# Kernel tuning notes

Measured on AMD Instinct MI355X. Metric: run time of the kernel, lower is better.

Reference implementation:

```python
import jax, jax.numpy as jnp
import numpy as np

B, N_HEADS, F_TOK = 8, 12, 768
GRID_H, GRID_W = 32, 32
N_TOK = 1 + GRID_H * GRID_W  # 1025 (readout token + patches)
F_HEAD = F_TOK // N_HEADS    # 64
NUM_DIST = (2 * GRID_H - 1) * (2 * GRID_W - 1) + 3  # 3972


def _build_relpos_index(gh, gw):
    # BEiT-style relative position index with 3 extra slots for the readout token
    coords = np.stack(np.meshgrid(np.arange(gh), np.arange(gw), indexing='ij'))  # (2, gh, gw)
    flat = coords.reshape(2, -1)                                                 # (2, gh*gw)
    rel = flat[:, :, None] - flat[:, None, :]                                    # (2, P, P)
    rel = rel.transpose(1, 2, 0).astype(np.int64)                                # (P, P, 2)
    rel[:, :, 0] += gh - 1
    rel[:, :, 1] += gw - 1
    rel[:, :, 0] *= 2 * gw - 1
    rpi = rel.sum(-1)                                                            # (P, P)
    n = 1 + gh * gw
    nd = (2 * gh - 1) * (2 * gw - 1) + 3
    idx = np.zeros((n, n), dtype=np.int32)
    idx[1:, 1:] = rpi
    idx[0, :] = nd - 3  # readout -> all
    idx[:, 0] = nd - 2  # all -> readout
    idx[0, 0] = nd - 1  # readout -> readout
    return idx


def setup_inputs() -> dict:
    key = jax.random.key(0)
    ks = jax.random.split(key, 7)
    tokens = jax.random.normal(ks[0], (B, N_TOK, F_TOK), dtype=jnp.float32)
    qkv_w = jax.random.normal(ks[1], (3 * F_TOK, F_TOK), dtype=jnp.float32) * 0.02
    q_bias = jax.random.normal(ks[2], (1, N_HEADS, 1, F_HEAD), dtype=jnp.float32) * 0.02
    v_bias = jax.random.normal(ks[3], (1, N_HEADS, 1, F_HEAD), dtype=jnp.float32) * 0.02
    relpos_table = jax.random.normal(ks[4], (NUM_DIST, N_HEADS), dtype=jnp.float32) * 0.02
    proj_w = jax.random.normal(ks[5], (F_TOK, F_TOK), dtype=jnp.float32) * 0.02
    proj_b = jax.random.normal(ks[6], (F_TOK,), dtype=jnp.float32) * 0.02
    relpos_index = jnp.asarray(_build_relpos_index(GRID_H, GRID_W))  # (N, N) int32
    return {
        'tokens': tokens, 'qkv_w': qkv_w, 'q_bias': q_bias, 'v_bias': v_bias,
        'relpos_table': relpos_table, 'proj_w': proj_w, 'proj_b': proj_b,
        'relpos_index': relpos_index, 'patch_h': GRID_H, 'patch_w': GRID_W,
    }


def reference(tokens, qkv_w, q_bias, v_bias, relpos_table, proj_w, proj_b,
              relpos_index, patch_h, patch_w):
    b, n, f_tok = tokens.shape
    # qkv projection (no bias): (B, N, 3F) -> (3, B, H, N, f)
    qkv = tokens @ qkv_w.T
    qkv = qkv.reshape(b, n, 3, N_HEADS, F_HEAD).transpose(2, 0, 3, 1, 4)
    q, k, v = qkv[0], qkv[1], qkv[2]
    q = (q + q_bias) * (F_HEAD ** -0.5)
    v = v + v_bias
    # attention scores: (B, H, N, N)
    attn = jnp.einsum('bhnf,bhmf->bhnm', q, k)
    # relative position bias gather: (N, N, H) -> (H, N, N)
    bias = relpos_table[relpos_index].transpose(2, 0, 1)
    attn = attn + bias[None]
    w = jax.nn.softmax(attn, axis=-1)
    out = jnp.einsum('bhnm,bhmf->bhnf', w, v)
    out = out.transpose(0, 2, 1, 3).reshape(b, n, N_HEADS * F_HEAD)
    return out @ proj_w.T + proj_b
```

## Files before the change

kernel.cpp:

```cpp
#include <hip/hip_runtime.h>

#define B_ 8
#define NH 12
#define NTOK 1025
#define FT 768
#define MROWS (B_*NTOK)
#define QPAD 1025
#define CH2 34
#define NQT 36
#define NTT 34
#define NDIST 3972
#define LOG2E 1.44269504089f

typedef __bf16 bf16x8 __attribute__((ext_vector_type(8)));
typedef __bf16 bf16x2 __attribute__((ext_vector_type(2)));
typedef float floatx4 __attribute__((ext_vector_type(4)));
typedef float floatx16 __attribute__((ext_vector_type(16)));
typedef int intx4 __attribute__((ext_vector_type(4)));

__device__ __forceinline__ void async_ld16(const void* gp, void* lp) {
  __builtin_amdgcn_global_load_lds(
      (const __attribute__((address_space(1))) void*)gp,
      (__attribute__((address_space(3))) void*)lp, 16, 0, 0);
}

__global__ __launch_bounds__(256) void cvt_bf16(const float* __restrict__ src,
                                                __bf16* __restrict__ dst, int n4) {
  int i = blockIdx.x * 256 + threadIdx.x;
  if (i >= n4) return;
  float4 v = ((const float4*)src)[i];
  __bf16 o[4] = {(__bf16)v.x, (__bf16)v.y, (__bf16)v.z, (__bf16)v.w};
  *(uint2*)(dst + 4 * (size_t)i) = *(uint2*)o;
}

__global__ __launch_bounds__(256) void table_prep(const float* __restrict__ table,
                                                  __bf16* __restrict__ tableT) {
  int i = blockIdx.x * 256 + threadIdx.x;
  if (i >= NH * NDIST) return;
  int h = i / NDIST, d = i - h * NDIST;
  tableT[i] = (__bf16)(table[(size_t)d * NH + h] * LOG2E);
}

__global__ __launch_bounds__(256) void bias_gather_t(
    const int* __restrict__ idx, const __bf16* __restrict__ tableT,
    __bf16* __restrict__ Bb) {
  __shared__ int ids_l[32][33];
  const int qt = blockIdx.x, tt = blockIdx.y;
  const int t = threadIdx.x;
  {
    const int row = t >> 3, c4 = (t & 7) * 4;
    int qrow = qt * 32 + row; if (qrow > NTOK - 1) qrow = NTOK - 1;
    const int* src = idx + (size_t)qrow * NTOK;
#pragma unroll
    for (int j = 0; j < 4; ++j) {
      int token = tt * 32 + c4 + j; if (token > NTOK - 1) token = NTOK - 1;
      ids_l[row][c4 + j] = src[token];
    }
  }
  __syncthreads();
  const int lane = t & 63, w = t >> 6;
  const int l31 = lane & 31, hb = lane >> 5;
  int ids[16]; bool ok[16];
#pragma unroll
  for (int j = 0; j < 16; ++j) {
    const int col = (j & 3) + 8 * (j >> 2) + 4 * hb;
    ok[j] = tt * 32 + col < NTOK;
    ids[j] = ids_l[l31][col];
  }
#pragma unroll
  for (int g = 0; g < 3; ++g) {
    const int h = w + g * 4;
    const __bf16* tb = tableT + (size_t)h * NDIST;
    __bf16 v[16] __attribute__((aligned(16)));
#pragma unroll
    for (int j = 0; j < 16; ++j)
      v[j] = ok[j] ? tb[ids[j]] : (__bf16)(-1e30f);
    uint4* dst = (uint4*)(Bb + (((size_t)h * NQT + qt) * NTT + tt) * 1024 + lane * 16);
    dst[0] = ((uint4*)v)[0];
    dst[1] = ((uint4*)v)[1];
  }
}

__device__ __forceinline__ void gemm256_pipe(
    const __bf16* __restrict__ A, const __bf16* __restrict__ W,
    int am0, int n0, __bf16* Lt, floatx4 acc[4][4]) {
  const int tid = threadIdx.x, wave = tid >> 6, lane = tid & 63;
  const int l = lane & 15, qd = lane >> 4;
  const int srow = lane >> 2, sg = lane & 3;
  const int swb = (sg ^ (srow & 3)) * 8;
  const int wr = wave >> 1, wc = wave & 1;

  const __bf16* gsrc[3];
  int gdst[3];
#pragma unroll
  for (int i = 0; i < 3; ++i) {
    const int g = wave * 3 + i;
    if (g < 16) {
      int row = am0 + g * 16 + srow; if (row > MROWS - 1) row = MROWS - 1;
      gsrc[i] = A + (size_t)row * FT + swb;
      gdst[i] = g * 512;
    } else {
      const int row = n0 + (g - 16) * 16 + srow;
      gsrc[i] = W + (size_t)row * FT + swb;
      gdst[i] = 8192 + (g - 16) * 512;
    }
  }
  const int fsw = (qd ^ (l & 3)) * 8;

  auto issue = [&](int k, int buf) {
    __bf16* base = Lt + buf * 12288;
#pragma unroll
    for (int i = 0; i < 3; ++i)
      async_ld16(gsrc[i] + k * 32, base + gdst[i]);
  };
  auto step = [&](int buf) {
    __builtin_amdgcn_s_barrier();
    const __bf16* ab = Lt + buf * 12288;
    const __bf16* bb = ab + 8192;
    bf16x8 aF[4], bF[4];
#pragma unroll
    for (int t = 0; t < 4; ++t)
      aF[t] = *(const bf16x8*)(ab + (wr * 64 + t * 16 + l) * 32 + fsw);
#pragma unroll
    for (int u = 0; u < 4; ++u)
      bF[u] = *(const bf16x8*)(bb + (wc * 64 + u * 16 + l) * 32 + fsw);
#pragma unroll
    for (int t = 0; t < 4; ++t)
#pragma unroll
      for (int u = 0; u < 4; ++u)
        acc[t][u] = __builtin_amdgcn_mfma_f32_16x16x32_bf16(aF[t], bF[u], acc[t][u], 0, 0, 0);
  };

  issue(0, 0);
  int b0 = 0;
  for (int k = 0; k < 24; ++k) {
    if (k < 23) {
      int b1 = b0 + 1; if (b1 == 3) b1 = 0;
      issue(k + 1, b1);
      __builtin_amdgcn_s_waitcnt(0x0F73);
    } else {
      __builtin_amdgcn_s_waitcnt(0x0F70);
    }
    step(b0);
    ++b0; if (b0 == 3) b0 = 0;
  }
}

__global__ __launch_bounds__(512, 4) void qkv_gemm256(
    const __bf16* __restrict__ tokens, const __bf16* __restrict__ qkvw,
    const float* __restrict__ qbias, const float* __restrict__ vbias,
    __bf16* __restrict__ Qb, __bf16* __restrict__ Kc, __bf16* __restrict__ Vc) {
  __shared__ __bf16 Lt[3 * 12288];
  const int u0 = blockIdx.x;
  const int c = u0 & 7, i0 = u0 >> 3;
  const int base = (c < 2) ? c * 75 : 150 + (c - 2) * 74;
  const int w = base + i0;
  const int mt = w / 18, ni = w % 18;
  const int am0 = mt * 256, n0 = ni * 128;
  const int tid = threadIdx.x, wave = tid >> 6, lane = tid & 63;
  const int l = lane & 15, qd = lane >> 4;
  const int wr = wave >> 1, wc = wave & 1;
  floatx4 acc[4][4];
#pragma unroll
  for (int t = 0; t < 4; ++t)
#pragma unroll
    for (int u = 0; u < 4; ++u) acc[t][u] = (floatx4){0.f, 0.f, 0.f, 0.f};
  gemm256_pipe(tokens, qkvw, am0, n0, Lt, acc);

  const int which = ni / 6;
  const int nrem0 = (ni - which * 6) * 128;
#pragma unroll
  for (int u = 0; u < 4; ++u) {
    const int rem = nrem0 + wc * 64 + u * 16 + l;
    const int h = rem >> 6, f = rem & 63;
    const float qb = (which == 0) ? qbias[h * 64 + f] : 0.f;
    const float vb = (which == 2) ? vbias[h * 64 + f] : 0.f;
#pragma unroll
    for (int t = 0; t < 4; ++t) {
      const int gmb = am0 + wr * 64 + t * 16 + qd * 4;
#pragma unroll
      for (int r = 0; r < 4; ++r) {
        const int gm = gmb + r;
        if (gm >= MROWS) continue;
        const int b = (int)(((unsigned)gm * 16369u) >> 24);
        const int tok = gm - b * 1025;
        const size_t bh = (size_t)(b * NH + h);
        const float v = acc[t][u][r];
        if (which == 0) {
          Qb[(bh * QPAD + tok) * 64 + f] = (__bf16)((v + qb) * (0.125f * LOG2E));
        } else if (which == 1) {
          const size_t e = (bh * CH2 + (tok >> 5)) * 2048 +
                           (f >> 3) * 256 + (tok & 31) * 8 + (f & 7);
          Kc[e] = (__bf16)v;
        } else {
          const size_t e = (bh * CH2 + (tok >> 5)) * 2048 +
                           (((tok >> 3) & 3) * 64 + f) * 8 + (tok & 7);
          Vc[e] = (__bf16)(v + vb);
        }
      }
    }
  }
}

__global__ __launch_bounds__(512, 4) void proj_gemm256(
    const __bf16* __restrict__ Ao, const __bf16* __restrict__ projw,
    const float* __restrict__ projb, float* __restrict__ out) {
  __shared__ __bf16 Lt[3 * 12288];
  const int u0 = blockIdx.x;
  const int c = u0 & 7, i0 = u0 >> 3;
  const int base = (c < 6) ? c * 25 : 150 + (c - 6) * 24;
  const int w = base + i0;
  const int mt = w / 6, ni = w % 6;
  const int am0 = mt * 256, n0 = ni * 128;
  const int tid = threadIdx.x, wave = tid >> 6, lane = tid & 63;
  const int l = lane & 15, qd = lane >> 4;
  const int wr = wave >> 1, wc = wave & 1;
  floatx4 acc[4][4];
#pragma unroll
  for (int t = 0; t < 4; ++t)
#pragma unroll
    for (int u = 0; u < 4; ++u) acc[t][u] = (floatx4){0.f, 0.f, 0.f, 0.f};
  gemm256_pipe(Ao, projw, am0, n0, Lt, acc);

#pragma unroll
  for (int u = 0; u < 4; ++u) {
    const int gn = n0 + wc * 64 + u * 16 + l;
    const float pb = projb[gn];
#pragma unroll
    for (int t = 0; t < 4; ++t) {
      const int gmb = am0 + wr * 64 + t * 16 + qd * 4;
#pragma unroll
      for (int r = 0; r < 4; ++r) {
        const int gm = gmb + r;
        if (gm < MROWS) out[(size_t)gm * FT + gn] = acc[t][u][r] + pb;
      }
    }
  }
}

__global__ __launch_bounds__(256) void attn_flash(
    const __bf16* __restrict__ Qb, const __bf16* __restrict__ Kc,
    const __bf16* __restrict__ Vc, const __bf16* __restrict__ Bb,
    __bf16* __restrict__ Ao) {
  __shared__ __bf16 Kl[3][4096], Vl[3][4096];
  const int bh = blockIdx.x;
  const int h = bh % NH, b = bh / NH;
  const int wave = threadIdx.x >> 6, lane = threadIdx.x & 63;
  const int l31 = lane & 31, hb = lane >> 5;
  const int qt = blockIdx.y * 4 + wave;
  int qrow = qt * 32 + l31; if (qrow > NTOK - 1) qrow = NTOK - 1;

  bf16x8 qf[4];
  {
    const __bf16* Qp = Qb + ((size_t)bh * QPAD + qrow) * 64 + hb * 8;
#pragma unroll
    for (int d = 0; d < 4; ++d) qf[d] = *(const bf16x8*)(Qp + d * 16);
  }

  floatx16 o0, o1;
#pragma unroll
  for (int j = 0; j < 16; ++j) { o0[j] = 0.f; o1[j] = 0.f; }
  float lsA = 0.f, lsB = 0.f;

  const int sw = wave & 1;
  const __bf16* Sg = ((wave < 2) ? Kc : Vc) + (size_t)bh * CH2 * 2048 +
                     sw * 2048 + lane * 8;
  __bf16* Sl0 = ((wave < 2) ? &Kl[0][0] : &Vl[0][0]) + sw * 2048;
  const __bf16* Bg = Bb + ((size_t)h * NQT + qt) * NTT * 1024 + lane * 16;

  auto issueS = [&](int c2, int buf) {
    const __bf16* src = Sg + (size_t)c2 * 4096;
    __bf16* dst = Sl0 + buf * 4096;
    async_ld16(src, dst);
    async_ld16(src + 512, dst + 512);
    async_ld16(src + 1024, dst + 1024);
    async_ld16(src + 1536, dst + 1536);
  };

  bf16x8 bA0, bA1, bA2, bA3, bB0, bB1, bB2, bB3;
  auto loadBA = [&](int c2) {
    const __bf16* p = Bg + (size_t)(2 * c2) * 1024;
    bA0 = *(const bf16x8*)(p);
    bA1 = *(const bf16x8*)(p + 8);
    bA2 = *(const bf16x8*)(p + 1024);
    bA3 = *(const bf16x8*)(p + 1032);
  };
  auto loadBB = [&](int c2) {
    const __bf16* p = Bg + (size_t)(2 * c2) * 1024;
    bB0 = *(const bf16x8*)(p);
    bB1 = *(const bf16x8*)(p + 8);
    bB2 = *(const bf16x8*)(p + 1024);
    bB3 = *(const bf16x8*)(p + 1032);
  };

  floatx16 st;
  auto qkHalf = [&](int buf, int th, bf16x8 c0, bf16x8 c1) {
    const __bf16* Kb = &Kl[buf][0] + th * 2048;
#pragma unroll
    for (int j = 0; j < 16; ++j) st[j] = (float)(j < 8 ? c0[j] : c1[j - 8]);
    __builtin_amdgcn_s_setprio(1);
#pragma unroll
    for (int dk = 0; dk < 4; ++dk) {
      bf16x8 a = *(const bf16x8*)(Kb + ((dk * 2 + hb) * 32 + l31) * 8);
      st = __builtin_amdgcn_mfma_f32_32x32x16_bf16(a, qf[dk], st, 0, 0, 0);
    }
    __builtin_amdgcn_s_setprio(0);
  };

  auto svHalf = [&](int buf, int th) {
    const __bf16* Vb = &Vl[buf][0] + th * 2048;
    float e[16];
#pragma unroll
    for (int j = 0; j < 16; ++j) e[j] = __builtin_amdgcn_exp2f(st[j]);
    lsA += ((e[0] + e[1]) + (e[2] + e[3])) + ((e[4] + e[5]) + (e[6] + e[7]));
    lsB += ((e[8] + e[9]) + (e[10] + e[11])) + ((e[12] + e[13]) + (e[14] + e[15]));
    int pk[8];
#pragma unroll
    for (int j2 = 0; j2 < 8; ++j2) {
      bf16x2 pr = {(__bf16)e[2 * j2], (__bf16)e[2 * j2 + 1]};
      pk[j2] = __builtin_bit_cast(int, pr);
    }
    __builtin_amdgcn_s_setprio(1);
#pragma unroll
    for (int ks = 0; ks < 2; ++ks) {
      const int r01a = pk[4 * ks + 0], r01b = pk[4 * ks + 1];
      const int r23a = pk[4 * ks + 2], r23b = pk[4 * ks + 3];
      const int t01a = __shfl_xor(r01a, 32), t01b = __shfl_xor(r01b, 32);
      const int t23a = __shfl_xor(r23a, 32), t23b = __shfl_xor(r23b, 32);
      intx4 fi;
      fi[0] = hb ? t23a : r01a;
      fi[1] = hb ? t23b : r01b;
      fi[2] = hb ? r23a : t01a;
      fi[3] = hb ? r23b : t01b;
      bf16x8 pb = __builtin_bit_cast(bf16x8, fi);
      bf16x8 va0 = *(const bf16x8*)(Vb + ((ks * 2 + hb) * 64 + l31) * 8);
      bf16x8 va1 = *(const bf16x8*)(Vb + ((ks * 2 + hb) * 64 + 32 + l31) * 8);
      o0 = __builtin_amdgcn_mfma_f32_32x32x16_bf16(va0, pb, o0, 0, 0, 0);
      o1 = __builtin_amdgcn_mfma_f32_32x32x16_bf16(va1, pb, o1, 0, 0, 0);
    }
    __builtin_amdgcn_s_setprio(0);
  };

  issueS(0, 0);
  loadBA(0);
  issueS(1, 1);
  loadBB(1);
  int bufc = 0;
  for (int ci = 0; ci < 8; ++ci) {
    const int c = 2 * ci;
    __builtin_amdgcn_s_waitcnt(0x0F78);
    __builtin_amdgcn_s_barrier();
    qkHalf(bufc, 0, bA0, bA1);
    { int pb_ = bufc + 2; if (pb_ >= 3) pb_ -= 3; issueS(c + 2, pb_); }
    svHalf(bufc, 0);
    qkHalf(bufc, 1, bA2, bA3);
    loadBA(c + 2);
    svHalf(bufc, 1);
    bufc = (bufc + 1 == 3) ? 0 : bufc + 1;
    __builtin_amdgcn_s_waitcnt(0x0F78);
    __builtin_amdgcn_s_barrier();
    qkHalf(bufc, 0, bB0, bB1);
    if (ci < 7) { int pb_ = bufc + 2; if (pb_ >= 3) pb_ -= 3; issueS(c + 3, pb_); }
    svHalf(bufc, 0);
    qkHalf(bufc, 1, bB2, bB3);
    if (ci < 7) loadBB(c + 3);
    svHalf(bufc, 1);
    bufc = (bufc + 1 == 3) ? 0 : bufc + 1;
  }
  __builtin_amdgcn_s_waitcnt(0x0F70);
  __builtin_amdgcn_s_barrier();
  qkHalf(bufc, 0, bA0, bA1);
  svHalf(bufc, 0);
  qkHalf(bufc, 1, bA2, bA3);
  svHalf(bufc, 1);

  const float ls = lsA + lsB;
  const float ltot = ls + __shfl_xor(ls, 32);
  const float rinv = 1.0f / ltot;
  const int tok = qt * 32 + l31;
  if (tok < NTOK) {
    __bf16* op = Ao + ((size_t)b * NTOK + tok) * FT + h * 64;
#pragma unroll
    for (int ft = 0; ft < 2; ++ft) {
#pragma unroll
      for (int jg = 0; jg < 4; ++jg) {
        const int f = ft * 32 + jg * 8 + hb * 4;
        __bf16 v4[4] __attribute__((aligned(8)));
#pragma unroll
        for (int q = 0; q < 4; ++q) {
          const float ov = ft ? o1[jg * 4 + q] : o0[jg * 4 + q];
          v4[q] = (__bf16)(ov * rinv);
        }
        *(uint2*)(op + f) = *(uint2*)v4;
      }
    }
  }
}

extern "C" void kernel_launch(void* const* d_in, const int* in_sizes, int n_in,
                              void* d_out, int out_size, void* d_ws, size_t ws_size,
                              hipStream_t stream) {
  (void)in_sizes; (void)n_in; (void)out_size; (void)ws_size;
  const float* tokens = (const float*)d_in[0];
  const float* qkvw   = (const float*)d_in[1];
  const float* qbias  = (const float*)d_in[2];
  const float* vbias  = (const float*)d_in[3];
  const float* table  = (const float*)d_in[4];
  const float* projw  = (const float*)d_in[5];
  const float* projb  = (const float*)d_in[6];
  const int*   rpidx  = (const int*)d_in[7];
  float* out = (float*)d_out;
  char* ws = (char*)d_ws;

  const size_t QBQ = (size_t)B_ * NH * QPAD * 64 * 2;
  const size_t KVB = (size_t)B_ * NH * CH2 * 2048 * 2;
  const size_t BBT = (size_t)NH * NQT * NTT * 1024 * 2;
  const size_t AOB = (size_t)MROWS * FT * 2;
  const size_t WQB = (size_t)3 * FT * FT * 2;
  const size_t WPB = (size_t)FT * FT * 2;
  __bf16* Qb = (__bf16*)(ws);
  __bf16* Kc = (__bf16*)(ws + QBQ);
  __bf16* Vc = (__bf16*)(ws + QBQ + KVB);
  __bf16* Bb = (__bf16*)(ws + QBQ + 2 * KVB);
  __bf16* Tb = (__bf16*)(ws + QBQ + 2 * KVB + BBT);
  __bf16* Ao = Tb;
  __bf16* Wq = (__bf16*)(ws + QBQ + 2 * KVB + BBT + AOB);
  __bf16* Wp = (__bf16*)(ws + QBQ + 2 * KVB + BBT + AOB + WQB);
  __bf16* Tt = (__bf16*)(ws + QBQ + 2 * KVB + BBT + AOB + WQB + WPB);

  cvt_bf16<<<(MROWS * FT / 4 + 255) / 256, 256, 0, stream>>>(tokens, Tb, MROWS * FT / 4);
  cvt_bf16<<<(3 * FT * FT / 4 + 255) / 256, 256, 0, stream>>>(qkvw, Wq, 3 * FT * FT / 4);
  cvt_bf16<<<(FT * FT / 4 + 255) / 256, 256, 0, stream>>>(projw, Wp, FT * FT / 4);
  table_prep<<<(NH * NDIST + 255) / 256, 256, 0, stream>>>(table, Tt);
  bias_gather_t<<<dim3(NQT, NTT), 256, 0, stream>>>(rpidx, Tt, Bb);
  qkv_gemm256<<<33 * 18, 512, 0, stream>>>(Tb, Wq, qbias, vbias, Qb, Kc, Vc);
  attn_flash<<<dim3(B_ * NH, 9), 256, 0, stream>>>(Qb, Kc, Vc, Bb, Ao);
  proj_gemm256<<<33 * 6, 512, 0, stream>>>(Ao, Wp, projb, out);
}
```

Before: 247.4 us.

## Fuse prep kernels, shrink GEMM and V LDS buffering to double-buffer

Merges the three bf16 conversion kernels and the table-prep kernel into one launch, which cuts launch overhead. Both GEMMs switch from triple-buffered to double-buffered LDS with a full wait before each step. The attention kernel keeps three K buffers but only two V buffers, and the V loader waves issue their next chunk after the barrier. Together these lower LDS use, which could allow more resident blocks, but they shorten the prefetch distance and may expose more memory latency.

```diff
diff --git a/kernel.cpp b/kernel.cpp
--- a/kernel.cpp
+++ b/kernel.cpp
@@ -24,21 +24,42 @@
       (__attribute__((address_space(3))) void*)lp, 16, 0, 0);
 }
 
-__global__ __launch_bounds__(256) void cvt_bf16(const float* __restrict__ src,
-                                                __bf16* __restrict__ dst, int n4) {
-  int i = blockIdx.x * 256 + threadIdx.x;
-  if (i >= n4) return;
-  float4 v = ((const float4*)src)[i];
-  __bf16 o[4] = {(__bf16)v.x, (__bf16)v.y, (__bf16)v.z, (__bf16)v.w};
-  *(uint2*)(dst + 4 * (size_t)i) = *(uint2*)o;
-}
-
-__global__ __launch_bounds__(256) void table_prep(const float* __restrict__ table,
-                                                  __bf16* __restrict__ tableT) {
-  int i = blockIdx.x * 256 + threadIdx.x;
-  if (i >= NH * NDIST) return;
-  int h = i / NDIST, d = i - h * NDIST;
-  tableT[i] = (__bf16)(table[(size_t)d * NH + h] * LOG2E);
+__global__ __launch_bounds__(256) void prep_fused(
+    const float* __restrict__ tokens, const float* __restrict__ qkvw,
+    const float* __restrict__ projw, const float* __restrict__ table,
+    __bf16* __restrict__ Tb, __bf16* __restrict__ Wq, __bf16* __restrict__ Wp,
+    __bf16* __restrict__ Tt) {
+  const int N1 = MROWS * FT / 4;
+  const int N2 = N1 + 3 * FT * FT / 4;
+  const int N3 = N2 + FT * FT / 4;
+  const int NT = NH * NDIST;
+  const int N4 = N3 + (NT + 3) / 4;
+  const int i = blockIdx.x * 256 + threadIdx.x;
+  if (i < N1) {
+    float4 v = ((const float4*)tokens)[i];
+    __bf16 o[4] = {(__bf16)v.x, (__bf16)v.y, (__bf16)v.z, (__bf16)v.w};
+    *(uint2*)(Tb + 4 * (size_t)i) = *(uint2*)o;
+  } else if (i < N2) {
+    const int j = i - N1;
+    float4 v = ((const float4*)qkvw)[j];
+    __bf16 o[4] = {(__bf16)v.x, (__bf16)v.y, (__bf16)v.z, (__bf16)v.w};
+    *(uint2*)(Wq + 4 * (size_t)j) = *(uint2*)o;
+  } else if (i < N3) {
+    const int j = i - N2;
+    float4 v = ((const float4*)projw)[j];
+    __bf16 o[4] = {(__bf16)v.x, (__bf16)v.y, (__bf16)v.z, (__bf16)v.w};
+    *(uint2*)(Wp + 4 * (size_t)j) = *(uint2*)o;
+  } else if (i < N4) {
+    const int base = (i - N3) * 4;
+#pragma unroll
+    for (int j = 0; j < 4; ++j) {
+      const int e = base + j;
+      if (e < NT) {
+        const int h = e / NDIST, d = e - h * NDIST;
+        Tt[e] = (__bf16)(table[(size_t)d * NH + h] * LOG2E);
+      }
+    }
+  }
 }
 
 __global__ __launch_bounds__(256) void bias_gather_t(
@@ -113,9 +134,13 @@
     for (int i = 0; i < 3; ++i)
       async_ld16(gsrc[i] + k * 32, base + gdst[i]);
   };
-  auto step = [&](int buf) {
+
+  issue(0, 0);
+  for (int k = 0; k < 24; ++k) {
+    __builtin_amdgcn_s_waitcnt(0x0F70);
     __builtin_amdgcn_s_barrier();
-    const __bf16* ab = Lt + buf * 12288;
+    if (k < 23) issue(k + 1, (k + 1) & 1);
+    const __bf16* ab = Lt + (k & 1) * 12288;
     const __bf16* bb = ab + 8192;
     bf16x8 aF[4], bF[4];
 #pragma unroll
@@ -129,20 +154,6 @@
 #pragma unroll
       for (int u = 0; u < 4; ++u)
         acc[t][u] = __builtin_amdgcn_mfma_f32_16x16x32_bf16(aF[t], bF[u], acc[t][u], 0, 0, 0);
-  };
-
-  issue(0, 0);
-  int b0 = 0;
-  for (int k = 0; k < 24; ++k) {
-    if (k < 23) {
-      int b1 = b0 + 1; if (b1 == 3) b1 = 0;
-      issue(k + 1, b1);
-      __builtin_amdgcn_s_waitcnt(0x0F73);
-    } else {
-      __builtin_amdgcn_s_waitcnt(0x0F70);
-    }
-    step(b0);
-    ++b0; if (b0 == 3) b0 = 0;
   }
 }
 
@@ -150,7 +161,7 @@
     const __bf16* __restrict__ tokens, const __bf16* __restrict__ qkvw,
     const float* __restrict__ qbias, const float* __restrict__ vbias,
     __bf16* __restrict__ Qb, __bf16* __restrict__ Kc, __bf16* __restrict__ Vc) {
-  __shared__ __bf16 Lt[3 * 12288];
+  __shared__ __bf16 Lt[2 * 12288];
   const int u0 = blockIdx.x;
   const int c = u0 & 7, i0 = u0 >> 3;
   const int base = (c < 2) ? c * 75 : 150 + (c - 2) * 74;
@@ -205,7 +216,7 @@
 __global__ __launch_bounds__(512, 4) void proj_gemm256(
     const __bf16* __restrict__ Ao, const __bf16* __restrict__ projw,
     const float* __restrict__ projb, float* __restrict__ out) {
-  __shared__ __bf16 Lt[3 * 12288];
+  __shared__ __bf16 Lt[2 * 12288];
   const int u0 = blockIdx.x;
   const int c = u0 & 7, i0 = u0 >> 3;
   const int base = (c < 6) ? c * 25 : 150 + (c - 6) * 24;
@@ -242,13 +253,15 @@
     const __bf16* __restrict__ Qb, const __bf16* __restrict__ Kc,
     const __bf16* __restrict__ Vc, const __bf16* __restrict__ Bb,
     __bf16* __restrict__ Ao) {
-  __shared__ __bf16 Kl[3][4096], Vl[3][4096];
+  __shared__ __bf16 Kl[3][4096], Vl[2][4096];
   const int bh = blockIdx.x;
   const int h = bh % NH, b = bh / NH;
   const int wave = threadIdx.x >> 6, lane = threadIdx.x & 63;
   const int l31 = lane & 31, hb = lane >> 5;
   const int qt = blockIdx.y * 4 + wave;
   int qrow = qt * 32 + l31; if (qrow > NTOK - 1) qrow = NTOK - 1;
+  const int wv = __builtin_amdgcn_readfirstlane(wave);
+  const bool isK = (wv < 2);
 
   bf16x8 qf[4];
   {
@@ -263,9 +276,8 @@
   float lsA = 0.f, lsB = 0.f;
 
   const int sw = wave & 1;
-  const __bf16* Sg = ((wave < 2) ? Kc : Vc) + (size_t)bh * CH2 * 2048 +
-                     sw * 2048 + lane * 8;
-  __bf16* Sl0 = ((wave < 2) ? &Kl[0][0] : &Vl[0][0]) + sw * 2048;
+  const __bf16* Sg = (isK ? Kc : Vc) + (size_t)bh * CH2 * 2048 + sw * 2048 + lane * 8;
+  __bf16* Sl0 = (isK ? &Kl[0][0] : &Vl[0][0]) + sw * 2048;
   const __bf16* Bg = Bb + ((size_t)h * NQT + qt) * NTT * 1024 + lane * 16;
 
   auto issueS = [&](int c2, int buf) {
@@ -294,8 +306,8 @@
   };
 
   floatx16 st;
-  auto qkHalf = [&](int buf, int th, bf16x8 c0, bf16x8 c1) {
-    const __bf16* Kb = &Kl[buf][0] + th * 2048;
+  auto qkHalf = [&](int kb, int th, bf16x8 c0, bf16x8 c1) {
+    const __bf16* Kb = &Kl[kb][0] + th * 2048;
 #pragma unroll
     for (int j = 0; j < 16; ++j) st[j] = (float)(j < 8 ? c0[j] : c1[j - 8]);
     __builtin_amdgcn_s_setprio(1);
@@ -307,8 +319,8 @@
     __builtin_amdgcn_s_setprio(0);
   };
 
-  auto svHalf = [&](int buf, int th) {
-    const __bf16* Vb = &Vl[buf][0] + th * 2048;
+  auto svHalf = [&](int vb, int th) {
+    const __bf16* Vb = &Vl[vb][0] + th * 2048;
     float e[16];
 #pragma unroll
     for (int j = 0; j < 16; ++j) e[j] = __builtin_amdgcn_exp2f(st[j]);
@@ -341,38 +353,44 @@
     __builtin_amdgcn_s_setprio(0);
   };
 
-  issueS(0, 0);
-  loadBA(0);
-  issueS(1, 1);
-  loadBB(1);
-  int bufc = 0;
+  if (isK) {
+    issueS(0, 0); loadBA(0); issueS(1, 1); loadBB(1);
+  } else {
+    issueS(0, 0); loadBA(0); loadBB(1);
+  }
+
+  int kb = 0;
   for (int ci = 0; ci < 8; ++ci) {
     const int c = 2 * ci;
-    __builtin_amdgcn_s_waitcnt(0x0F78);
+    if (isK) __builtin_amdgcn_s_waitcnt(0x0F78);
+    else     __builtin_amdgcn_s_waitcnt(0x0F74);
     __builtin_amdgcn_s_barrier();
-    qkHalf(bufc, 0, bA0, bA1);
-    { int pb_ = bufc + 2; if (pb_ >= 3) pb_ -= 3; issueS(c + 2, pb_); }
-    svHalf(bufc, 0);
-    qkHalf(bufc, 1, bA2, bA3);
+    if (!isK) issueS(c + 1, 1);
+    qkHalf(kb, 0, bA0, bA1);
+    if (isK) { int nb = kb + 2; if (nb >= 3) nb -= 3; issueS(c + 2, nb); }
+    svHalf(0, 0);
+    qkHalf(kb, 1, bA2, bA3);
     loadBA(c + 2);
-    svHalf(bufc, 1);
-    bufc = (bufc + 1 == 3) ? 0 : bufc + 1;
-    __builtin_amdgcn_s_waitcnt(0x0F78);
+    svHalf(0, 1);
+    kb = (kb + 1 == 3) ? 0 : kb + 1;
+    if (isK) __builtin_amdgcn_s_waitcnt(0x0F78);
+    else     __builtin_amdgcn_s_waitcnt(0x0F74);
     __builtin_amdgcn_s_barrier();
-    qkHalf(bufc, 0, bB0, bB1);
-    if (ci < 7) { int pb_ = bufc + 2; if (pb_ >= 3) pb_ -= 3; issueS(c + 3, pb_); }
-    svHalf(bufc, 0);
-    qkHalf(bufc, 1, bB2, bB3);
+    if (!isK) issueS(c + 2, 0);
+    qkHalf(kb, 0, bB0, bB1);
+    if (isK && ci < 7) { int nb = kb + 2; if (nb >= 3) nb -= 3; issueS(c + 3, nb); }
+    svHalf(1, 0);
+    qkHalf(kb, 1, bB2, bB3);
     if (ci < 7) loadBB(c + 3);
-    svHalf(bufc, 1);
-    bufc = (bufc + 1 == 3) ? 0 : bufc + 1;
+    svHalf(1, 1);
+    kb = (kb + 1 == 3) ? 0 : kb + 1;
   }
   __builtin_amdgcn_s_waitcnt(0x0F70);
   __builtin_amdgcn_s_barrier();
-  qkHalf(bufc, 0, bA0, bA1);
-  svHalf(bufc, 0);
-  qkHalf(bufc, 1, bA2, bA3);
-  svHalf(bufc, 1);
+  qkHalf(kb, 0, bA0, bA1);
+  svHalf(0, 0);
+  qkHalf(kb, 1, bA2, bA3);
+  svHalf(0, 1);
 
   const float ls = lsA + lsB;
   const float ltot = ls + __shfl_xor(ls, 32);
@@ -428,10 +446,9 @@
   __bf16* Wp = (__bf16*)(ws + QBQ + 2 * KVB + BBT + AOB + WQB);
   __bf16* Tt = (__bf16*)(ws + QBQ + 2 * KVB + BBT + AOB + WQB + WPB);
 
-  cvt_bf16<<<(MROWS * FT / 4 + 255) / 256, 256, 0, stream>>>(tokens, Tb, MROWS * FT / 4);
-  cvt_bf16<<<(3 * FT * FT / 4 + 255) / 256, 256, 0, stream>>>(qkvw, Wq, 3 * FT * FT / 4);
-  cvt_bf16<<<(FT * FT / 4 + 255) / 256, 256, 0, stream>>>(projw, Wp, FT * FT / 4);
-  table_prep<<<(NH * NDIST + 255) / 256, 256, 0, stream>>>(table, Tt);
+  const int NPREP = MROWS * FT / 4 + 3 * FT * FT / 4 + FT * FT / 4 + (NH * NDIST + 3) / 4;
+  prep_fused<<<(NPREP + 255) / 256, 256, 0, stream>>>(tokens, qkvw, projw, table,
+                                                      Tb, Wq, Wp, Tt);
   bias_gather_t<<<dim3(NQT, NTT), 256, 0, stream>>>(rpidx, Tt, Bb);
   qkv_gemm256<<<33 * 18, 512, 0, stream>>>(Tb, Wq, qbias, vbias, Qb, Kc, Vc);
   attn_flash<<<dim3(B_ * NH, 9), 256, 0, stream>>>(Qb, Kc, Vc, Bb, Ao);
```

New measurement: 250.8 us. About the same (+1.4%).
